# Kernel optimization log

Measured on AMD Instinct MI355X. Metric: run time of the kernel, lower is better.

The kernel has to match this reference:

```python
import jax, jax.numpy as jnp
import numpy as np

B, S, D = 2, 2048, 1024
H = 16
HD = D // H  # head_dim = 64
EPS = 1e-5


def _layernorm(x, g, b):
    mu = jnp.mean(x, axis=-1, keepdims=True)
    var = jnp.mean(jnp.square(x - mu), axis=-1, keepdims=True)
    return (x - mu) * jax.lax.rsqrt(var + EPS) * g + b


def setup_inputs() -> dict:
    key = jax.random.key(0)
    ks = jax.random.split(key, 6)
    # Xavier-normal-ish init for projection weights (torch Linear layout: [out, in])
    std = float(np.sqrt(2.0 / (D + D)))
    return {
        "query": jax.random.normal(ks[0], (B, S, D), dtype=jnp.float32),
        "q_w": jax.random.normal(ks[1], (D, D), dtype=jnp.float32) * std,
        "q_b": jnp.zeros((D,), jnp.float32),
        "k_w": jax.random.normal(ks[2], (D, D), dtype=jnp.float32) * std,
        "k_b": jnp.zeros((D,), jnp.float32),
        "v_w": jax.random.normal(ks[3], (D, D), dtype=jnp.float32) * std,
        "v_b": jnp.zeros((D,), jnp.float32),
        "o_w": jax.random.normal(ks[4], (D, D), dtype=jnp.float32) * std,
        "o_b": jnp.zeros((D,), jnp.float32),
        "q_ln_g": jnp.ones((HD,), jnp.float32),
        "q_ln_b": jnp.zeros((HD,), jnp.float32),
        "k_ln_g": jnp.ones((HD,), jnp.float32),
        "k_ln_b": jnp.zeros((HD,), jnp.float32),
    }


def reference(query, q_w, q_b, k_w, k_b, v_w, v_b, o_w, o_b,
              q_ln_g, q_ln_b, k_ln_g, k_ln_b) -> jnp.ndarray:
    # Self-attention: key = value = query
    q = query @ q_w.T + q_b           # [B, S, D]
    k = query @ k_w.T + k_b
    v = query @ v_w.T + v_b
    q = q.reshape(B, S, H, HD)
    k = k.reshape(B, S, H, HD)
    v = v.reshape(B, S, H, HD)
    # Per-head QK LayerNorm (ViT-22B stabilization)
    q = _layernorm(q, q_ln_g, q_ln_b)
    k = _layernorm(k, k_ln_g, k_ln_b)
    scale = 1.0 / jnp.sqrt(jnp.asarray(HD, q.dtype))
    attn = jnp.einsum("bqhd,bkhd->bhqk", q, k) * scale  # [B, H, Sq, Skv]
    attn = jax.nn.softmax(attn, axis=-1)
    out = jnp.einsum("bhqk,bkhd->bqhd", attn, v)        # [B, Sq, H, HD]
    out = out.reshape(B, S, D)
    return out @ o_w.T + o_b
```

## Files before the change

### kernel.cpp

```cpp
#include <hip/hip_runtime.h>
#include <hip/hip_bf16.h>

typedef float f32x4 __attribute__((ext_vector_type(4)));
typedef __bf16 bf16x8 __attribute__((ext_vector_type(8)));
typedef unsigned short ushort8 __attribute__((ext_vector_type(8)));

#define SEQ 2048
#define LOG2E 1.4426950408889634f

__device__ __forceinline__ unsigned short f2bf(float f) {
    unsigned int u = __builtin_bit_cast(unsigned int, f);
    unsigned int r = (u + 0x7FFFu + ((u >> 16) & 1u)) >> 16;
    return (unsigned short)r;
}

__device__ __forceinline__ void gload_lds16(const unsigned short* g, unsigned short* l) {
    __builtin_amdgcn_global_load_lds(
        (const __attribute__((address_space(1))) unsigned int*)g,
        (__attribute__((address_space(3))) unsigned int*)l, 16, 0, 0);
}

__global__ __launch_bounds__(256) void conv_bf16(
    const float* __restrict__ s0, const float* __restrict__ s1,
    const float* __restrict__ s2, const float* __restrict__ s3,
    const float* __restrict__ s4,
    unsigned short* __restrict__ d0, unsigned short* __restrict__ d1,
    unsigned short* __restrict__ d2, unsigned short* __restrict__ d3,
    unsigned short* __restrict__ d4)
{
    const int seg = blockIdx.y;
    const float* s = seg == 0 ? s0 : seg == 1 ? s1 : seg == 2 ? s2 : seg == 3 ? s3 : s4;
    unsigned short* d = seg == 0 ? d0 : seg == 1 ? d1 : seg == 2 ? d2 : seg == 3 ? d3 : d4;
    const int n = seg == 0 ? (4096 * 1024) : (1024 * 1024);
    const int i = (blockIdx.x * 256 + threadIdx.x) * 8;
    if (i >= n) return;
    float4 a = *(const float4*)(s + i);
    float4 b = *(const float4*)(s + i + 4);
    ushort8 o;
    o[0] = f2bf(a.x); o[1] = f2bf(a.y); o[2] = f2bf(a.z); o[3] = f2bf(a.w);
    o[4] = f2bf(b.x); o[5] = f2bf(b.y); o[6] = f2bf(b.z); o[7] = f2bf(b.w);
    *(ushort8*)(d + i) = o;
}

__global__ __launch_bounds__(256) void gemm_bf16(
    const unsigned short* __restrict__ A,
    const unsigned short* __restrict__ W0, const unsigned short* __restrict__ W1,
    const unsigned short* __restrict__ W2,
    const float* __restrict__ b0, const float* __restrict__ b1, const float* __restrict__ b2,
    const float* __restrict__ ln_g0, const float* __restrict__ ln_b0,
    const float* __restrict__ ln_g1, const float* __restrict__ ln_b1,
    unsigned short* __restrict__ qn, unsigned short* __restrict__ kn,
    unsigned short* __restrict__ vt,
    float* __restrict__ Cout, int fixed_mode)
{
    const int z = fixed_mode < 0 ? (int)blockIdx.z : fixed_mode;
    const unsigned short* W = (z == 1) ? W1 : (z == 2) ? W2 : W0;
    const float* bias = (z == 1) ? b1 : (z == 2) ? b2 : b0;

    const int bm = blockIdx.y * 128;
    const int bn = blockIdx.x * 128;

    __shared__ unsigned short As[128 * 64];
    __shared__ unsigned short Bs[128 * 64];

    const int t    = threadIdx.x;
    const int lane = t & 63;
    const int wid  = t >> 6;
    const int l15  = lane & 15;
    const int lhi  = lane >> 4;
    const int wm   = (wid >> 1) * 64;
    const int wn   = (wid & 1) * 64;

    const int schunk = (lane & 7) ^ ((lane >> 3) & 7);
    const unsigned short* Ag = A + (size_t)(bm + (lane >> 3)) * 1024 + schunk * 8;
    const unsigned short* Wg = W + (size_t)(bn + (lane >> 3)) * 1024 + schunk * 8;

    f32x4 acc[4][4];
#pragma unroll
    for (int i = 0; i < 4; ++i)
#pragma unroll
        for (int j = 0; j < 4; ++j) acc[i][j] = (f32x4)0.f;

    const int phase = (blockIdx.x * 3 + blockIdx.y * 5 + z * 11) & 15;

#pragma unroll 1
    for (int it = 0; it < 16; ++it) {
        const int kt = ((it + phase) & 15) * 64;
        __syncthreads();
#pragma unroll
        for (int c = 0; c < 4; ++c) {
            const int ch = wid * 4 + c;
            gload_lds16(Ag + (size_t)ch * 8 * 1024 + kt, &As[ch * 512]);
            gload_lds16(Wg + (size_t)ch * 8 * 1024 + kt, &Bs[ch * 512]);
        }
        __syncthreads();
#pragma unroll
        for (int kk = 0; kk < 2; ++kk) {
            const int rchunk = ((kk * 4 + lhi) ^ (l15 & 7)) * 8;
            bf16x8 af[4], bw[4];
#pragma unroll
            for (int mi = 0; mi < 4; ++mi)
                af[mi] = __builtin_bit_cast(bf16x8,
                    *(const ushort8*)(&As[(wm + mi * 16 + l15) * 64 + rchunk]));
#pragma unroll
            for (int ni = 0; ni < 4; ++ni)
                bw[ni] = __builtin_bit_cast(bf16x8,
                    *(const ushort8*)(&Bs[(wn + ni * 16 + l15) * 64 + rchunk]));
#pragma unroll
            for (int mi = 0; mi < 4; ++mi)
#pragma unroll
                for (int ni = 0; ni < 4; ++ni)
                    acc[mi][ni] = __builtin_amdgcn_mfma_f32_16x16x32_bf16(af[mi], bw[ni], acc[mi][ni], 0, 0, 0);
        }
    }
    __syncthreads();

    if (z == 3) {
#pragma unroll
        for (int ni = 0; ni < 4; ++ni) {
            const int col = bn + wn + ni * 16 + l15;
            const float bv = bias[col];
#pragma unroll
            for (int mi = 0; mi < 4; ++mi) {
                const int row = bm + wm + mi * 16 + lhi * 4;
#pragma unroll
                for (int r = 0; r < 4; ++r)
                    Cout[(size_t)(row + r) * 1024 + col] = acc[mi][ni][r] + bv;
            }
        }
        return;
    }

    unsigned short* stg = ((wid & 2) ? Bs : As) + (wid & 1) * 4096;
    const int h = (bn + wn) >> 6;

    if (z == 2) {
        float biasv[4];
#pragma unroll
        for (int ni = 0; ni < 4; ++ni) biasv[ni] = bias[bn + wn + ni * 16 + l15];
#pragma unroll
        for (int mi = 0; mi < 4; ++mi)
#pragma unroll
            for (int ni = 0; ni < 4; ++ni)
#pragma unroll
                for (int r = 0; r < 4; ++r)
                    stg[(ni * 16 + l15) * 64 + 32 * (mi >> 1) + lhi * 8 + 2 * r + (mi & 1)] =
                        f2bf(acc[mi][ni][r] + biasv[ni]);
        __builtin_amdgcn_s_waitcnt(0);
        const int srow0 = bm + wm;
        const int b = srow0 >> 11, sbase = srow0 & 2047;
#pragma unroll
        for (int i = 0; i < 8; ++i) {
            const int dl = i * 8 + (lane >> 3);
            const ushort8 v = *(const ushort8*)(&stg[dl * 64 + (((lane & 7) ^ (dl & 7)) * 8)]);
            *(ushort8*)(&vt[((size_t)((b * 16 + h) * 64 + dl)) * 2048 + sbase + (lane & 7) * 8]) = v;
        }
        return;
    }

    const float* g  = (z == 0) ? ln_g0 : ln_g1;
    const float* bb = (z == 0) ? ln_b0 : ln_b1;
    unsigned short* outp = (z == 0) ? qn : kn;
    const float scale = (z == 0) ? 0.125f * LOG2E : 1.0f;
    const int sxor = (z == 1) ? 7 : 0;
    float gv[4], bbv[4], biasv[4];
#pragma unroll
    for (int ni = 0; ni < 4; ++ni) {
        const int d = ni * 16 + l15;
        gv[ni] = g[d]; bbv[ni] = bb[d]; biasv[ni] = bias[bn + wn + d];
    }
#pragma unroll
    for (int mi = 0; mi < 4; ++mi) {
#pragma unroll
        for (int r = 0; r < 4; ++r) {
            float x0 = acc[mi][0][r] + biasv[0];
            float x1 = acc[mi][1][r] + biasv[1];
            float x2 = acc[mi][2][r] + biasv[2];
            float x3 = acc[mi][3][r] + biasv[3];
            float sum = (x0 + x1) + (x2 + x3);
#pragma unroll
            for (int off = 1; off < 16; off <<= 1) sum += __shfl_xor(sum, off);
            const float mean = sum * (1.f / 64.f);
            const float d0 = x0 - mean, d1 = x1 - mean, d2 = x2 - mean, d3 = x3 - mean;
            float vs = (d0 * d0 + d1 * d1) + (d2 * d2 + d3 * d3);
#pragma unroll
            for (int off = 1; off < 16; off <<= 1) vs += __shfl_xor(vs, off);
            const float rstd = rsqrtf(vs * (1.f / 64.f) + 1e-5f);
            const int rl = mi * 16 + lhi * 4 + r;
            stg[rl * 64 +  0 + l15] = f2bf((d0 * rstd * gv[0] + bbv[0]) * scale);
            stg[rl * 64 + 16 + l15] = f2bf((d1 * rstd * gv[1] + bbv[1]) * scale);
            stg[rl * 64 + 32 + l15] = f2bf((d2 * rstd * gv[2] + bbv[2]) * scale);
            stg[rl * 64 + 48 + l15] = f2bf((d3 * rstd * gv[3] + bbv[3]) * scale);
        }
    }
    __builtin_amdgcn_s_waitcnt(0);
#pragma unroll
    for (int i = 0; i < 8; ++i) {
        const int rl  = i * 8 + (lane >> 3);
        const int srow = bm + wm + rl;
        const int b = srow >> 11, s = srow & 2047;
        const ushort8 v = *(const ushort8*)(&stg[rl * 64 + (((lane & 7) ^ (rl & sxor)) * 8)]);
        *(ushort8*)(&outp[((size_t)((b * 16 + h) * 2048 + s)) * 64 + (lane & 7) * 8]) = v;
    }
}

__global__ __launch_bounds__(256) void gemm_out(
    const unsigned short* __restrict__ A,
    const unsigned short* __restrict__ W,
    const float* __restrict__ bias,
    float* __restrict__ Cout)
{
    const int bm = blockIdx.x * 64;
    const int bn = blockIdx.y * 128;

    __shared__ unsigned short As[64 * 64];
    __shared__ unsigned short Bs[128 * 64];

    const int t    = threadIdx.x;
    const int lane = t & 63;
    const int wid  = t >> 6;
    const int l15  = lane & 15;
    const int lhi  = lane >> 4;
    const int wm   = (wid >> 1) * 32;
    const int wn   = (wid & 1) * 64;

    const int schunk = (lane & 7) ^ ((lane >> 3) & 7);
    const unsigned short* Ag = A + (size_t)(bm + (lane >> 3)) * 1024 + schunk * 8;
    const unsigned short* Wg = W + (size_t)(bn + (lane >> 3)) * 1024 + schunk * 8;

    f32x4 acc[2][4];
#pragma unroll
    for (int i = 0; i < 2; ++i)
#pragma unroll
        for (int j = 0; j < 4; ++j) acc[i][j] = (f32x4)0.f;

    const int phase = (blockIdx.x * 3 + blockIdx.y * 5) & 15;

#pragma unroll 1
    for (int it = 0; it < 16; ++it) {
        const int kt = ((it + phase) & 15) * 64;
        __syncthreads();
#pragma unroll
        for (int c = 0; c < 2; ++c) {
            const int ch = wid * 2 + c;
            gload_lds16(Ag + (size_t)ch * 8 * 1024 + kt, &As[ch * 512]);
        }
#pragma unroll
        for (int c = 0; c < 4; ++c) {
            const int ch = wid * 4 + c;
            gload_lds16(Wg + (size_t)ch * 8 * 1024 + kt, &Bs[ch * 512]);
        }
        __syncthreads();
#pragma unroll
        for (int kk = 0; kk < 2; ++kk) {
            const int rchunk = ((kk * 4 + lhi) ^ (l15 & 7)) * 8;
            bf16x8 af[2], bw[4];
#pragma unroll
            for (int mi = 0; mi < 2; ++mi)
                af[mi] = __builtin_bit_cast(bf16x8,
                    *(const ushort8*)(&As[(wm + mi * 16 + l15) * 64 + rchunk]));
#pragma unroll
            for (int ni = 0; ni < 4; ++ni)
                bw[ni] = __builtin_bit_cast(bf16x8,
                    *(const ushort8*)(&Bs[(wn + ni * 16 + l15) * 64 + rchunk]));
#pragma unroll
            for (int mi = 0; mi < 2; ++mi)
#pragma unroll
                for (int ni = 0; ni < 4; ++ni)
                    acc[mi][ni] = __builtin_amdgcn_mfma_f32_16x16x32_bf16(af[mi], bw[ni], acc[mi][ni], 0, 0, 0);
        }
    }

#pragma unroll
    for (int ni = 0; ni < 4; ++ni) {
        const int col = bn + wn + ni * 16 + l15;
        const float bv = bias[col];
#pragma unroll
        for (int mi = 0; mi < 2; ++mi) {
            const int row = bm + wm + mi * 16 + lhi * 4;
#pragma unroll
            for (int r = 0; r < 4; ++r)
                Cout[(size_t)(row + r) * 1024 + col] = acc[mi][ni][r] + bv;
        }
    }
}

__global__ __launch_bounds__(512, 4) void attn(
    const unsigned short* __restrict__ qn, const unsigned short* __restrict__ kn,
    const unsigned short* __restrict__ vt, unsigned short* __restrict__ o)
{
    __shared__ unsigned short Ks[4][64 * 64];
    __shared__ unsigned short Vs[4][64 * 64];
    __shared__ unsigned short Ps[128 * 64];

    const int tid  = threadIdx.x;
    const int lane = tid & 63;
    const int w    = tid >> 6;
    const int l15  = lane & 15;
    const int lhi  = lane >> 4;

    const int bh = blockIdx.x;
    const int q0 = blockIdx.y * 128;

    const unsigned short* qrp = qn + ((size_t)bh * SEQ + q0 + w * 16 + l15) * 64 + lhi * 8;
    const bf16x8 aq0 = __builtin_bit_cast(bf16x8, *(const ushort8*)(qrp));
    const bf16x8 aq1 = __builtin_bit_cast(bf16x8, *(const ushort8*)(qrp + 32));

    const unsigned short* kg = kn + ((size_t)bh * SEQ + w * 8 + (lane >> 3)) * 64 + (lane & 7) * 8;
    const unsigned short* vg = vt + ((size_t)bh * 64 + w * 8 + (lane >> 3)) * 2048 + (lane & 7) * 8;

    f32x4 oacc[4];
#pragma unroll
    for (int nd = 0; nd < 4; ++nd) oacc[nd] = (f32x4)0.f;
    float l_part[4];
#pragma unroll
    for (int i = 0; i < 4; ++i) l_part[i] = 0.f;
    f32x4 mneg = (f32x4)100.f;

    f32x4 sacc[4];

    auto QK = [&](const unsigned short* kb) {
        __builtin_amdgcn_s_setprio(1);
#pragma unroll
        for (int ni = 0; ni < 4; ++ni) {
            const int krow = ni * 16 + l15;
            const bf16x8 bk = __builtin_bit_cast(bf16x8,
                *(const ushort8*)(&kb[krow * 64 + ((lhi ^ (krow & 7)) * 8)]));
            sacc[ni] = __builtin_amdgcn_mfma_f32_16x16x32_bf16(aq0, bk, mneg, 0, 0, 0);
        }
#pragma unroll
        for (int ni = 0; ni < 4; ++ni) {
            const int krow = ni * 16 + l15;
            const bf16x8 bk = __builtin_bit_cast(bf16x8,
                *(const ushort8*)(&kb[krow * 64 + (((4 + lhi) ^ (krow & 7)) * 8)]));
            sacc[ni] = __builtin_amdgcn_mfma_f32_16x16x32_bf16(aq1, bk, sacc[ni], 0, 0, 0);
        }
        __builtin_amdgcn_s_setprio(0);
    };

    gload_lds16(kg,                    &Ks[0][w * 512]);
    gload_lds16(vg,                    &Vs[0][w * 512]);
    gload_lds16(kg + (size_t)64 * 64,  &Ks[1][w * 512]);
    gload_lds16(vg + 64,               &Vs[1][w * 512]);
    __builtin_amdgcn_sched_barrier(0);
    asm volatile("s_waitcnt vmcnt(2)" ::: "memory");
    asm volatile("s_barrier" ::: "memory");
    QK(&Ks[0][0]);

#pragma unroll 4
    for (int t = 0; t < 32; ++t) {
        if (t < 30) {
            gload_lds16(kg + (size_t)(t + 2) * 64 * 64, &Ks[(t + 2) & 3][w * 512]);
            gload_lds16(vg + (t + 2) * 64,              &Vs[(t + 2) & 3][w * 512]);
        }
        __builtin_amdgcn_sched_barrier(0);

        float tmax[4];
#pragma unroll
        for (int r = 0; r < 4; ++r)
            tmax[r] = fmaxf(fmaxf(fmaxf(sacc[0][r], sacc[1][r]), sacc[2][r]), sacc[3][r]);
        const float dmax = fmaxf(fmaxf(fmaxf(tmax[0], tmax[1]), tmax[2]), tmax[3]);
        if (!__all(dmax <= 8.0f)) {
#pragma unroll
            for (int r = 0; r < 4; ++r) {
                float tm = tmax[r];
#pragma unroll
                for (int off = 1; off < 16; off <<= 1) tm = fmaxf(tm, __shfl_xor(tm, off));
                const float delta = fmaxf(tm, 0.f);
                const float alpha = __builtin_amdgcn_exp2f(-delta);
                mneg[r] -= delta;
                l_part[r] *= alpha;
#pragma unroll
                for (int nd = 0; nd < 4; ++nd) oacc[nd][r] *= alpha;
#pragma unroll
                for (int ni = 0; ni < 4; ++ni) sacc[ni][r] -= delta;
            }
        }
#pragma unroll
        for (int r = 0; r < 4; ++r) {
            const float p0 = __builtin_amdgcn_exp2f(sacc[0][r]);
            const float p1 = __builtin_amdgcn_exp2f(sacc[1][r]);
            const float p2 = __builtin_amdgcn_exp2f(sacc[2][r]);
            const float p3 = __builtin_amdgcn_exp2f(sacc[3][r]);
            l_part[r] += (p0 + p1) + (p2 + p3);
            unsigned int pk0, pk1;
            asm("v_cvt_pk_bf16_f32 %0, %1, %2" : "=v"(pk0) : "v"(p0), "v"(p1));
            asm("v_cvt_pk_bf16_f32 %0, %1, %2" : "=v"(pk1) : "v"(p2), "v"(p3));
            const int prow = w * 16 + lhi * 4 + r;
            const int rs7  = prow & 7;
            *(unsigned int*)(&Ps[prow * 64 + (((l15 >> 2) ^ rs7) * 8) + 2 * (l15 & 3)]) = pk0;
            *(unsigned int*)(&Ps[prow * 64 + (((4 + (l15 >> 2)) ^ rs7) * 8) + 2 * (l15 & 3)]) = pk1;
        }

        if (t < 31) {
            if (t < 30) { asm volatile("s_waitcnt vmcnt(2)" ::: "memory"); }
            else        { asm volatile("s_waitcnt vmcnt(0)" ::: "memory"); }
            asm volatile("s_barrier" ::: "memory");
            QK(&Ks[(t + 1) & 3][0]);
        }

        __builtin_amdgcn_s_setprio(1);
#pragma unroll
        for (int kk = 0; kk < 2; ++kk) {
            const int arow = w * 16 + l15;
            const bf16x8 ap = __builtin_bit_cast(bf16x8,
                *(const ushort8*)(&Ps[arow * 64 + (((kk * 4 + lhi) ^ (arow & 7)) * 8)]));
#pragma unroll
            for (int nd = 0; nd < 4; ++nd) {
                const int vrow = nd * 16 + l15;
                const bf16x8 bv = __builtin_bit_cast(bf16x8,
                    *(const ushort8*)(&Vs[t & 3][vrow * 64 + (((kk * 4 + lhi) ^ (vrow & 7)) * 8)]));
                oacc[nd] = __builtin_amdgcn_mfma_f32_16x16x32_bf16(ap, bv, oacc[nd], 0, 0, 0);
            }
        }
        __builtin_amdgcn_s_setprio(0);
    }

    const int b = bh >> 4, h = bh & 15;
#pragma unroll
    for (int r = 0; r < 4; ++r) {
        float ls = l_part[r];
#pragma unroll
        for (int off = 1; off < 16; off <<= 1) ls += __shfl_xor(ls, off);
        const float inv = 1.f / ls;
        const int qrow = q0 + w * 16 + lhi * 4 + r;
        const size_t base = ((size_t)(b * SEQ + qrow) * 16 + h) * 64;
#pragma unroll
        for (int nd = 0; nd < 4; ++nd)
            o[base + nd * 16 + l15] = f2bf(oacc[nd][r] * inv);
    }
}

extern "C" void kernel_launch(void* const* d_in, const int* in_sizes, int n_in,
                              void* d_out, int out_size, void* d_ws, size_t ws_size,
                              hipStream_t stream)
{
    const float* query  = (const float*)d_in[0];
    const float* q_w    = (const float*)d_in[1];
    const float* q_b    = (const float*)d_in[2];
    const float* k_w    = (const float*)d_in[3];
    const float* k_b    = (const float*)d_in[4];
    const float* v_w    = (const float*)d_in[5];
    const float* v_b    = (const float*)d_in[6];
    const float* o_w    = (const float*)d_in[7];
    const float* o_b    = (const float*)d_in[8];
    const float* q_ln_g = (const float*)d_in[9];
    const float* q_ln_b = (const float*)d_in[10];
    const float* k_ln_g = (const float*)d_in[11];
    const float* k_ln_b = (const float*)d_in[12];

    char* ws = (char*)d_ws;
    unsigned short* qbf = (unsigned short*)(ws);
    unsigned short* wq  = (unsigned short*)(ws + (8ull  << 20));
    unsigned short* wk  = (unsigned short*)(ws + (10ull << 20));
    unsigned short* wv  = (unsigned short*)(ws + (12ull << 20));
    unsigned short* wo  = (unsigned short*)(ws + (14ull << 20));
    unsigned short* qnb = (unsigned short*)(ws + (16ull << 20));
    unsigned short* knb = (unsigned short*)(ws + (24ull << 20));
    unsigned short* vtb = (unsigned short*)(ws + (32ull << 20));
    unsigned short* ofb = (unsigned short*)(ws + (40ull << 20));

    conv_bf16<<<dim3(2048, 5), 256, 0, stream>>>(query, q_w, k_w, v_w, o_w,
                                                 qbf, wq, wk, wv, wo);

    dim3 g1(8, 32, 3);
    gemm_bf16<<<g1, 256, 0, stream>>>(qbf, wq, wk, wv, q_b, k_b, v_b,
                                      q_ln_g, q_ln_b, k_ln_g, k_ln_b,
                                      qnb, knb, vtb, nullptr, -1);

    dim3 g3(32, 16);
    attn<<<g3, 512, 0, stream>>>(qnb, knb, vtb, ofb);

    dim3 g4(64, 8);
    gemm_out<<<g4, 256, 0, stream>>>(ofb, wo, o_b, (float*)d_out);
}
```

Before: 124.6 us.

## Double-buffer LDS tiles in projection GEMMs and swap block raster order

Both the QKV projection GEMM and the output projection GEMM now use two LDS buffers. The next K-tile's global-to-LDS loads are issued right after the barrier, so they overlap with the MFMA work on the current tile, and one barrier per iteration is dropped. The per-block K-phase staggering is removed, and the QKV grid is transposed so blockIdx.x walks M instead of N, which changes L2 reuse order. The cost is double the LDS per block, which may cut occupancy, and losing the staggered K-start may raise memory-channel contention.

```diff
diff --git a/kernel.cpp b/kernel.cpp
--- a/kernel.cpp
+++ b/kernel.cpp
@@ -57,11 +57,11 @@
     const unsigned short* W = (z == 1) ? W1 : (z == 2) ? W2 : W0;
     const float* bias = (z == 1) ? b1 : (z == 2) ? b2 : b0;
 
-    const int bm = blockIdx.y * 128;
-    const int bn = blockIdx.x * 128;
-
-    __shared__ unsigned short As[128 * 64];
-    __shared__ unsigned short Bs[128 * 64];
+    const int bm = blockIdx.x * 128;
+    const int bn = blockIdx.y * 128;
+
+    __shared__ unsigned short As[2][128 * 64];
+    __shared__ unsigned short Bs[2][128 * 64];
 
     const int t    = threadIdx.x;
     const int lane = t & 63;
@@ -81,19 +81,27 @@
 #pragma unroll
         for (int j = 0; j < 4; ++j) acc[i][j] = (f32x4)0.f;
 
-    const int phase = (blockIdx.x * 3 + blockIdx.y * 5 + z * 11) & 15;
-
-#pragma unroll 1
+#pragma unroll
+    for (int c = 0; c < 4; ++c) {
+        const int ch = wid * 4 + c;
+        gload_lds16(Ag + (size_t)ch * 8 * 1024, &As[0][ch * 512]);
+        gload_lds16(Wg + (size_t)ch * 8 * 1024, &Bs[0][ch * 512]);
+    }
+
+#pragma unroll 2
     for (int it = 0; it < 16; ++it) {
-        const int kt = ((it + phase) & 15) * 64;
         __syncthreads();
-#pragma unroll
-        for (int c = 0; c < 4; ++c) {
-            const int ch = wid * 4 + c;
-            gload_lds16(Ag + (size_t)ch * 8 * 1024 + kt, &As[ch * 512]);
-            gload_lds16(Wg + (size_t)ch * 8 * 1024 + kt, &Bs[ch * 512]);
-        }
-        __syncthreads();
+        if (it < 15) {
+            const int kt = (it + 1) * 64;
+#pragma unroll
+            for (int c = 0; c < 4; ++c) {
+                const int ch = wid * 4 + c;
+                gload_lds16(Ag + (size_t)ch * 8 * 1024 + kt, &As[(it + 1) & 1][ch * 512]);
+                gload_lds16(Wg + (size_t)ch * 8 * 1024 + kt, &Bs[(it + 1) & 1][ch * 512]);
+            }
+        }
+        const unsigned short* Ab = &As[it & 1][0];
+        const unsigned short* Bb = &Bs[it & 1][0];
 #pragma unroll
         for (int kk = 0; kk < 2; ++kk) {
             const int rchunk = ((kk * 4 + lhi) ^ (l15 & 7)) * 8;
@@ -101,11 +109,11 @@
 #pragma unroll
             for (int mi = 0; mi < 4; ++mi)
                 af[mi] = __builtin_bit_cast(bf16x8,
-                    *(const ushort8*)(&As[(wm + mi * 16 + l15) * 64 + rchunk]));
+                    *(const ushort8*)(&Ab[(wm + mi * 16 + l15) * 64 + rchunk]));
 #pragma unroll
             for (int ni = 0; ni < 4; ++ni)
                 bw[ni] = __builtin_bit_cast(bf16x8,
-                    *(const ushort8*)(&Bs[(wn + ni * 16 + l15) * 64 + rchunk]));
+                    *(const ushort8*)(&Bb[(wn + ni * 16 + l15) * 64 + rchunk]));
 #pragma unroll
             for (int mi = 0; mi < 4; ++mi)
 #pragma unroll
@@ -131,7 +139,7 @@
         return;
     }
 
-    unsigned short* stg = ((wid & 2) ? Bs : As) + (wid & 1) * 4096;
+    unsigned short* stg = ((wid & 2) ? &Bs[0][0] : &As[0][0]) + (wid & 1) * 4096;
     const int h = (bn + wn) >> 6;
 
     if (z == 2) {
@@ -213,8 +221,8 @@
     const int bm = blockIdx.x * 64;
     const int bn = blockIdx.y * 128;
 
-    __shared__ unsigned short As[64 * 64];
-    __shared__ unsigned short Bs[128 * 64];
+    __shared__ unsigned short As[2][64 * 64];
+    __shared__ unsigned short Bs[2][128 * 64];
 
     const int t    = threadIdx.x;
     const int lane = t & 63;
@@ -234,23 +242,35 @@
 #pragma unroll
         for (int j = 0; j < 4; ++j) acc[i][j] = (f32x4)0.f;
 
-    const int phase = (blockIdx.x * 3 + blockIdx.y * 5) & 15;
-
-#pragma unroll 1
+#pragma unroll
+    for (int c = 0; c < 2; ++c) {
+        const int ch = wid * 2 + c;
+        gload_lds16(Ag + (size_t)ch * 8 * 1024, &As[0][ch * 512]);
+    }
+#pragma unroll
+    for (int c = 0; c < 4; ++c) {
+        const int ch = wid * 4 + c;
+        gload_lds16(Wg + (size_t)ch * 8 * 1024, &Bs[0][ch * 512]);
+    }
+
+#pragma unroll 2
     for (int it = 0; it < 16; ++it) {
-        const int kt = ((it + phase) & 15) * 64;
         __syncthreads();
-#pragma unroll
-        for (int c = 0; c < 2; ++c) {
-            const int ch = wid * 2 + c;
-            gload_lds16(Ag + (size_t)ch * 8 * 1024 + kt, &As[ch * 512]);
-        }
-#pragma unroll
-        for (int c = 0; c < 4; ++c) {
-            const int ch = wid * 4 + c;
-            gload_lds16(Wg + (size_t)ch * 8 * 1024 + kt, &Bs[ch * 512]);
-        }
-        __syncthreads();
+        if (it < 15) {
+            const int kt = (it + 1) * 64;
+#pragma unroll
+            for (int c = 0; c < 2; ++c) {
+                const int ch = wid * 2 + c;
+                gload_lds16(Ag + (size_t)ch * 8 * 1024 + kt, &As[(it + 1) & 1][ch * 512]);
+            }
+#pragma unroll
+            for (int c = 0; c < 4; ++c) {
+                const int ch = wid * 4 + c;
+                gload_lds16(Wg + (size_t)ch * 8 * 1024 + kt, &Bs[(it + 1) & 1][ch * 512]);
+            }
+        }
+        const unsigned short* Ab = &As[it & 1][0];
+        const unsigned short* Bb = &Bs[it & 1][0];
 #pragma unroll
         for (int kk = 0; kk < 2; ++kk) {
             const int rchunk = ((kk * 4 + lhi) ^ (l15 & 7)) * 8;
@@ -258,11 +278,11 @@
 #pragma unroll
             for (int mi = 0; mi < 2; ++mi)
                 af[mi] = __builtin_bit_cast(bf16x8,
-                    *(const ushort8*)(&As[(wm + mi * 16 + l15) * 64 + rchunk]));
+                    *(const ushort8*)(&Ab[(wm + mi * 16 + l15) * 64 + rchunk]));
 #pragma unroll
             for (int ni = 0; ni < 4; ++ni)
                 bw[ni] = __builtin_bit_cast(bf16x8,
-                    *(const ushort8*)(&Bs[(wn + ni * 16 + l15) * 64 + rchunk]));
+                    *(const ushort8*)(&Bb[(wn + ni * 16 + l15) * 64 + rchunk]));
 #pragma unroll
             for (int mi = 0; mi < 2; ++mi)
 #pragma unroll
@@ -463,7 +483,7 @@
     conv_bf16<<<dim3(2048, 5), 256, 0, stream>>>(query, q_w, k_w, v_w, o_w,
                                                  qbf, wq, wk, wv, wo);
 
-    dim3 g1(8, 32, 3);
+    dim3 g1(32, 8, 3);
     gemm_bf16<<<g1, 256, 0, stream>>>(qbf, wq, wk, wv, q_b, k_b, v_b,
                                       q_ln_g, q_ln_b, k_ln_g, k_ln_b,
                                       qnb, knb, vtb, nullptr, -1);
```

Result: faster. 118.2 us (median of 2 runs) (-5.1%).
